# Kernel tuning notes

Measured on AMD Instinct MI355X. Metric: run time of the kernel, lower is better.

## Reference

```python
import jax, jax.numpy as jnp
import numpy as np

INPUT_DIM = 1024
OUTPUT_DIM = 512
N_QUBITS = 12
DEPTH = 8
BATCH = 32768
LN_EPS = 1e-5
NOISE = 0.01


def setup_inputs() -> dict:
    key = jax.random.key(0)
    ks = jax.random.split(key, 12)
    inp = {
        "x": jax.random.normal(ks[0], (BATCH, INPUT_DIM), dtype=jnp.float32),
        "w_in": jax.random.normal(ks[1], (N_QUBITS, INPUT_DIM), dtype=jnp.float32) * 0.03,
        "b_in": jnp.zeros((N_QUBITS,), jnp.float32),
        "ln_g": jnp.ones((N_QUBITS,), jnp.float32),
        "ln_b": jnp.zeros((N_QUBITS,), jnp.float32),
        "rot": jax.random.normal(ks[2], (DEPTH, N_QUBITS, 3), dtype=jnp.float32) * 0.1,
        "ent": jax.random.normal(ks[3], (DEPTH, N_QUBITS - 1), dtype=jnp.float32) * 0.1,
        "w1": jax.random.normal(ks[4], (N_QUBITS, N_QUBITS), dtype=jnp.float32) * 0.3,
        "b1": jnp.zeros((N_QUBITS,), jnp.float32),
        "w2": jax.random.normal(ks[5], (OUTPUT_DIM, N_QUBITS), dtype=jnp.float32) * 0.3,
        "b2": jnp.zeros((OUTPUT_DIM,), jnp.float32),
        "meas_basis": jax.random.normal(ks[6], (N_QUBITS,), dtype=jnp.float32) * 0.1,
    }
    return inp


def _entangle(state, c):
    # c: sigmoid(ent[layer]) shape [n-1]. Effective (traced) torch semantics:
    # out[i]   = s[i]*(1-c_i)   + s[i+1]*c_i     for i in 0..n-2
    # out[n-1] = s[n-1]*(1-c_{n-2}) + s[n-2]*c_{n-2}
    left = state[:, :-1] * (1.0 - c) + state[:, 1:] * c          # [B, n-1]
    last = state[:, -1] * (1.0 - c[-1]) + state[:, -2] * c[-1]   # [B]
    return jnp.concatenate([left, last[:, None]], axis=1)


def reference(x, w_in, b_in, ln_g, ln_b, rot, ent, w1, b1, w2, b2, meas_basis):
    # input layer + layernorm + tanh
    h = x @ w_in.T + b_in                                   # [B, n]
    mu = jnp.mean(h, axis=-1, keepdims=True)
    var = jnp.mean((h - mu) ** 2, axis=-1, keepdims=True)
    h = (h - mu) * jax.lax.rsqrt(var + LN_EPS) * ln_g + ln_b
    h = jnp.tanh(h)

    encoded = h * jnp.float32(np.pi)
    state = jnp.zeros_like(encoded)
    for layer in range(DEPTH):
        rx = encoded + rot[layer, :, 0]
        state = state * jnp.cos(rx * 0.5) + jnp.sin(rot[layer, :, 1] * 0.5)
        state = state * jnp.cos(rot[layer, :, 2] * 0.5)     # Re(exp(i*rz/2))
        if layer < DEPTH - 1:
            state = _entangle(state, jax.nn.sigmoid(ent[layer]))

    # measurement: basis rotation + gaussian noise + tanh
    measured = state * jnp.tanh(meas_basis)
    noise = jax.random.normal(jax.random.key(1234), measured.shape, dtype=measured.dtype) * NOISE
    measured = jnp.tanh(measured + noise)

    # output MLP
    out = jax.nn.relu(measured @ w1.T + b1) @ w2.T + b2     # [B, OUTPUT_DIM]
    return out
```

## Files before the change

kernel.cpp:

```cpp
#include <hip/hip_runtime.h>
#include <cstdint>
#include <cstddef>


__device__ __forceinline__ uint32_t rotl32(uint32_t x, int r) {
  return (x << r) | (x >> (32 - r));
}

__device__ __forceinline__ void threefry2x32(uint32_t k0, uint32_t k1,
                                             uint32_t& x0, uint32_t& x1) {
  const uint32_t k2 = k0 ^ k1 ^ 0x1BD11BDAu;
  x0 += k0; x1 += k1;
#define TF_R(r) { x0 += x1; x1 = rotl32(x1, (r)); x1 ^= x0; }
  TF_R(13) TF_R(15) TF_R(26) TF_R(6)
  x0 += k1; x1 += k2 + 1u;
  TF_R(17) TF_R(29) TF_R(16) TF_R(24)
  x0 += k2; x1 += k0 + 2u;
  TF_R(13) TF_R(15) TF_R(26) TF_R(6)
  x0 += k0; x1 += k1 + 3u;
  TF_R(17) TF_R(29) TF_R(16) TF_R(24)
  x0 += k1; x1 += k2 + 4u;
  TF_R(13) TF_R(15) TF_R(26) TF_R(6)
  x0 += k2; x1 += k0 + 5u;
#undef TF_R
}

__device__ __forceinline__ float erfinv_xla(float x) {
  float w = -log1pf(-x * x);
  float p;
  if (w < 5.0f) {
    w -= 2.5f;
    p = 2.81022636e-08f;
    p = fmaf(p, w, 3.43273939e-07f);
    p = fmaf(p, w, -3.5233877e-06f);
    p = fmaf(p, w, -4.39150654e-06f);
    p = fmaf(p, w, 0.00021858087f);
    p = fmaf(p, w, -0.00125372503f);
    p = fmaf(p, w, -0.00417768164f);
    p = fmaf(p, w, 0.246640727f);
    p = fmaf(p, w, 1.50140941f);
  } else {
    w = sqrtf(w) - 3.0f;
    p = -0.000200214257f;
    p = fmaf(p, w, 0.000100950558f);
    p = fmaf(p, w, 0.00134934322f);
    p = fmaf(p, w, -0.00367342844f);
    p = fmaf(p, w, 0.00573950773f);
    p = fmaf(p, w, -0.0076224613f);
    p = fmaf(p, w, 0.00943887047f);
    p = fmaf(p, w, 1.00167406f);
    p = fmaf(p, w, 2.83297682f);
  }
  return p * x;
}

__global__ __launch_bounds__(256, 3)
void qnn_gemm_in(const float* __restrict__ x, const float* __restrict__ w_in,
                 const float* __restrict__ b_in, float* __restrict__ h) {
  __shared__ float wl[12 * 1024];
  {
    const float4* ws = (const float4*)w_in;
    float4* wd = (float4*)wl;
#pragma unroll
    for (int j = 0; j < 12; ++j) wd[threadIdx.x + 256 * j] = ws[threadIdx.x + 256 * j];
  }
  __syncthreads();

  const int wave = threadIdx.x >> 6;
  const int lane = threadIdx.x & 63;
  const int r    = lane >> 4;
  const int kc   = lane & 15;

  float bq[12];
#pragma unroll
  for (int q = 0; q < 12; ++q) bq[q] = b_in[q];

  for (int it = 0; it < 4; ++it) {
    const int row = (blockIdx.x << 6) + (it << 4) + (wave << 2) + r;
    const float4* xr = (const float4*)(x + (size_t)row * 1024);

    float acc[12];
#pragma unroll
    for (int q = 0; q < 12; ++q) acc[q] = 0.0f;

#pragma unroll 4
    for (int ks = 0; ks < 16; ++ks) {
      const float4 xv = xr[(ks << 4) + kc];
#pragma unroll
      for (int q = 0; q < 12; ++q) {
        const float4 wv = *(const float4*)&wl[q * 1024 + (ks << 6) + (kc << 2)];
        acc[q] += xv.x * wv.x + xv.y * wv.y + xv.z * wv.z + xv.w * wv.w;
      }
    }

#pragma unroll
    for (int q = 0; q < 12; ++q) {
      float v = acc[q];
      v += __shfl_xor(v, 1);
      v += __shfl_xor(v, 2);
      v += __shfl_xor(v, 4);
      v += __shfl_xor(v, 8);
      acc[q] = v + bq[q];
    }
    if (kc == 0) {
      float* hp = h + (size_t)row * 12;
      *(float4*)(hp + 0) = make_float4(acc[0], acc[1], acc[2], acc[3]);
      *(float4*)(hp + 4) = make_float4(acc[4], acc[5], acc[6], acc[7]);
      *(float4*)(hp + 8) = make_float4(acc[8], acc[9], acc[10], acc[11]);
    }
  }
}

__global__ __launch_bounds__(256, 2)
void qnn_tail(const float* __restrict__ h_in,
              const float* __restrict__ ln_g, const float* __restrict__ ln_b,
              const float* __restrict__ rot,  const float* __restrict__ ent,
              const float* __restrict__ w1,   const float* __restrict__ b1,
              const float* __restrict__ w2,   const float* __restrict__ b2,
              const float* __restrict__ meas, float* __restrict__ out) {
  __shared__ float w2s[512 * 12];
  __shared__ float b2s[512];
  __shared__ float hid[64 * 12];
  __shared__ float rot0[8][12], sr1[8][12], cr2[8][12], cen[8][12];
  __shared__ float tmb[12], w1s[144], b1s[12];

  const int t = threadIdx.x;

  {
    const float4* s = (const float4*)w2;
    float4* d = (float4*)w2s;
#pragma unroll
    for (int j = 0; j < 6; ++j) d[t + 256 * j] = s[t + 256 * j];
    if (t < 128) ((float4*)b2s)[t] = ((const float4*)b2)[t];
    if (t < 96) {
      const int l = t / 12, q = t % 12, base = (l * 12 + q) * 3;
      rot0[l][q] = rot[base + 0];
      sr1[l][q]  = sinf(rot[base + 1] * 0.5f);
      cr2[l][q]  = cosf(rot[base + 2] * 0.5f);
    }
    if (t >= 128 && t < 216) {
      const int i = t - 128, l = i / 11, q = i % 11;
      cen[l][q] = 1.0f / (1.0f + expf(-ent[l * 11 + q]));
    }
    if (t >= 216 && t < 228) tmb[t - 216] = tanhf(meas[t - 216]);
    if (t >= 228 && t < 240) b1s[t - 228] = b1[t - 228];
    if (t < 144) w1s[t] = w1[t];
  }
  __syncthreads();

  const int wave = t >> 6, lane = t & 63;
  if (lane < 16) {
    const int rl  = (wave << 4) + lane;
    const int row = (blockIdx.x << 6) + rl;

    const float* hp = h_in + (size_t)row * 12;
    const float4 a0 = *(const float4*)(hp + 0);
    const float4 a1 = *(const float4*)(hp + 4);
    const float4 a2 = *(const float4*)(hp + 8);
    float hv[12] = {a0.x, a0.y, a0.z, a0.w, a1.x, a1.y, a1.z, a1.w,
                    a2.x, a2.y, a2.z, a2.w};

    float s = 0.0f;
#pragma unroll
    for (int q = 0; q < 12; ++q) s += hv[q];
    const float mu = s / 12.0f;
    float var = 0.0f;
#pragma unroll
    for (int q = 0; q < 12; ++q) { const float d = hv[q] - mu; var += d * d; }
    var /= 12.0f;
    const float inv = 1.0f / sqrtf(var + 1e-5f);

    float enc[12];
#pragma unroll
    for (int q = 0; q < 12; ++q) {
      const float n = (hv[q] - mu) * inv * ln_g[q] + ln_b[q];
      enc[q] = tanhf(n) * 3.14159265358979f;
    }

    float st[12];
#pragma unroll
    for (int q = 0; q < 12; ++q) st[q] = 0.0f;
#pragma unroll
    for (int l = 0; l < 8; ++l) {
#pragma unroll
      for (int q = 0; q < 12; ++q) {
        const float rx = enc[q] + rot0[l][q];
        st[q] = st[q] * cosf(rx * 0.5f) + sr1[l][q];
        st[q] *= cr2[l][q];
      }
      if (l < 7) {
        float ns[12];
#pragma unroll
        for (int i = 0; i < 11; ++i) {
          const float c = cen[l][i];
          ns[i] = st[i] * (1.0f - c) + st[i + 1] * c;
        }
        { const float c = cen[l][10]; ns[11] = st[11] * (1.0f - c) + st[10] * c; }
#pragma unroll
        for (int q = 0; q < 12; ++q) st[q] = ns[q];
      }
    }

    const uint32_t base = (uint32_t)row * 12u;
    float m[12];
#pragma unroll
    for (int q = 0; q < 12; ++q) {
      uint32_t x0 = 0u;
      uint32_t x1 = base + (uint32_t)q;
      threefry2x32(0u, 1234u, x0, x1);
      const uint32_t bits = x0 ^ x1;
      const float u01 = __uint_as_float((bits >> 9) | 0x3F800000u) - 1.0f;
      float u = u01 * 2.0f + (-0.99999994f);
      u = fmaxf(-0.99999994f, u);
      const float nrm = 1.41421356237f * erfinv_xla(u);
      m[q] = tanhf(st[q] * tmb[q] + nrm * 0.01f);
    }

    float* hd = &hid[rl * 12];
#pragma unroll
    for (int j = 0; j < 12; ++j) {
      float a = b1s[j];
#pragma unroll
      for (int q = 0; q < 12; ++q) a = fmaf(m[q], w1s[j * 12 + q], a);
      hd[j] = fmaxf(a, 0.0f);
    }
  }
  __syncthreads();

  float wa[12], wb[12];
#pragma unroll
  for (int q = 0; q < 12; ++q) {
    wa[q] = w2s[t * 12 + q];
    wb[q] = w2s[(t + 256) * 12 + q];
  }
  const float ba = b2s[t], bb = b2s[t + 256];
  float* ob = out + (size_t)blockIdx.x * 64 * 512;
  for (int rr = 0; rr < 64; ++rr) {
    const float4 h0 = *(const float4*)&hid[rr * 12 + 0];
    const float4 h1 = *(const float4*)&hid[rr * 12 + 4];
    const float4 h2 = *(const float4*)&hid[rr * 12 + 8];
    const float hvv[12] = {h0.x, h0.y, h0.z, h0.w, h1.x, h1.y, h1.z, h1.w,
                           h2.x, h2.y, h2.z, h2.w};
    float a = ba, b = bb;
#pragma unroll
    for (int q = 0; q < 12; ++q) {
      a = fmaf(hvv[q], wa[q], a);
      b = fmaf(hvv[q], wb[q], b);
    }
    ob[rr * 512 + t] = a;
    ob[rr * 512 + 256 + t] = b;
  }
}

extern "C" void kernel_launch(void* const* d_in, const int* in_sizes, int n_in,
                              void* d_out, int out_size, void* d_ws, size_t ws_size,
                              hipStream_t stream) {
  const float* x    = (const float*)d_in[0];
  const float* w_in = (const float*)d_in[1];
  const float* b_in = (const float*)d_in[2];
  const float* ln_g = (const float*)d_in[3];
  const float* ln_b = (const float*)d_in[4];
  const float* rot  = (const float*)d_in[5];
  const float* ent  = (const float*)d_in[6];
  const float* w1   = (const float*)d_in[7];
  const float* b1   = (const float*)d_in[8];
  const float* w2   = (const float*)d_in[9];
  const float* b2   = (const float*)d_in[10];
  const float* mb   = (const float*)d_in[11];
  float* outp = (float*)d_out;
  float* h    = (float*)d_ws;

  qnn_gemm_in<<<512, 256, 0, stream>>>(x, w_in, b_in, h);
  qnn_tail<<<512, 256, 0, stream>>>(h, ln_g, ln_b, rot, ent, w1, b1, w2, b2, mb, outp);
}
```

Baseline: 292.4 us.

## Parallelize tail per-qubit across lanes and software-pipeline input GEMM loads

The input GEMM now uses 512-thread blocks and issues its x loads early into two alternating register buffers, so global loads overlap the FMA work. The tail kernel switches from one thread per row, with only 16 of 64 lanes active, to 16 lanes per row with one qubit per lane. LayerNorm sums and the entanglement neighbour exchange use wavefront shuffles, and the blocks are halved to 32 rows with twice as many blocks. This targets idle lanes and serial per-row work in the tail, at the cost of extra shuffles, four padded idle lanes per group, and higher register pressure from the prefetch buffers.

```diff
diff --git a/kernel.cpp b/kernel.cpp
--- a/kernel.cpp
+++ b/kernel.cpp
@@ -54,7 +54,7 @@
   return p * x;
 }
 
-__global__ __launch_bounds__(256, 3)
+__global__ __launch_bounds__(512, 4)
 void qnn_gemm_in(const float* __restrict__ x, const float* __restrict__ w_in,
                  const float* __restrict__ b_in, float* __restrict__ h) {
   __shared__ float wl[12 * 1024];
@@ -62,7 +62,7 @@
     const float4* ws = (const float4*)w_in;
     float4* wd = (float4*)wl;
 #pragma unroll
-    for (int j = 0; j < 12; ++j) wd[threadIdx.x + 256 * j] = ws[threadIdx.x + 256 * j];
+    for (int j = 0; j < 6; ++j) wd[threadIdx.x + 512 * j] = ws[threadIdx.x + 512 * j];
   }
   __syncthreads();
 
@@ -75,21 +75,61 @@
 #pragma unroll
   for (int q = 0; q < 12; ++q) bq[q] = b_in[q];
 
-  for (int it = 0; it < 4; ++it) {
-    const int row = (blockIdx.x << 6) + (it << 4) + (wave << 2) + r;
+#pragma unroll
+  for (int it = 0; it < 2; ++it) {
+    const int row = (blockIdx.x << 6) + (wave << 3) + (it << 2) + r;
     const float4* xr = (const float4*)(x + (size_t)row * 1024);
 
+    float4 A[4], B[4];
+#pragma unroll
+    for (int i = 0; i < 4; ++i) A[i] = xr[((0 + i) << 4) + kc];
+#pragma unroll
+    for (int i = 0; i < 4; ++i) B[i] = xr[((4 + i) << 4) + kc];
+
     float acc[12];
 #pragma unroll
     for (int q = 0; q < 12; ++q) acc[q] = 0.0f;
 
-#pragma unroll 4
-    for (int ks = 0; ks < 16; ++ks) {
-      const float4 xv = xr[(ks << 4) + kc];
+#pragma unroll
+    for (int i = 0; i < 4; ++i) {
+      const int ks = i;
 #pragma unroll
       for (int q = 0; q < 12; ++q) {
         const float4 wv = *(const float4*)&wl[q * 1024 + (ks << 6) + (kc << 2)];
-        acc[q] += xv.x * wv.x + xv.y * wv.y + xv.z * wv.z + xv.w * wv.w;
+        acc[q] += A[i].x * wv.x + A[i].y * wv.y + A[i].z * wv.z + A[i].w * wv.w;
+      }
+    }
+#pragma unroll
+    for (int i = 0; i < 4; ++i) A[i] = xr[((8 + i) << 4) + kc];
+
+#pragma unroll
+    for (int i = 0; i < 4; ++i) {
+      const int ks = 4 + i;
+#pragma unroll
+      for (int q = 0; q < 12; ++q) {
+        const float4 wv = *(const float4*)&wl[q * 1024 + (ks << 6) + (kc << 2)];
+        acc[q] += B[i].x * wv.x + B[i].y * wv.y + B[i].z * wv.z + B[i].w * wv.w;
+      }
+    }
+#pragma unroll
+    for (int i = 0; i < 4; ++i) B[i] = xr[((12 + i) << 4) + kc];
+
+#pragma unroll
+    for (int i = 0; i < 4; ++i) {
+      const int ks = 8 + i;
+#pragma unroll
+      for (int q = 0; q < 12; ++q) {
+        const float4 wv = *(const float4*)&wl[q * 1024 + (ks << 6) + (kc << 2)];
+        acc[q] += A[i].x * wv.x + A[i].y * wv.y + A[i].z * wv.z + A[i].w * wv.w;
+      }
+    }
+#pragma unroll
+    for (int i = 0; i < 4; ++i) {
+      const int ks = 12 + i;
+#pragma unroll
+      for (int q = 0; q < 12; ++q) {
+        const float4 wv = *(const float4*)&wl[q * 1024 + (ks << 6) + (kc << 2)];
+        acc[q] += B[i].x * wv.x + B[i].y * wv.y + B[i].z * wv.z + B[i].w * wv.w;
       }
     }
 
@@ -111,7 +151,7 @@
   }
 }
 
-__global__ __launch_bounds__(256, 2)
+__global__ __launch_bounds__(256, 4)
 void qnn_tail(const float* __restrict__ h_in,
               const float* __restrict__ ln_g, const float* __restrict__ ln_b,
               const float* __restrict__ rot,  const float* __restrict__ ent,
@@ -120,9 +160,9 @@
               const float* __restrict__ meas, float* __restrict__ out) {
   __shared__ float w2s[512 * 12];
   __shared__ float b2s[512];
-  __shared__ float hid[64 * 12];
-  __shared__ float rot0[8][12], sr1[8][12], cr2[8][12], cen[8][12];
-  __shared__ float tmb[12], w1s[144], b1s[12];
+  __shared__ float hid[32 * 12];
+  __shared__ float rot0s[8 * 16], sr1s[8 * 16], cr2s[8 * 16], cens[8 * 16];
+  __shared__ float tmbs[16], w1T[12 * 16], b1s[16], lgs[16], lbs[16];
 
   const int t = threadIdx.x;
 
@@ -134,96 +174,19 @@
     if (t < 128) ((float4*)b2s)[t] = ((const float4*)b2)[t];
     if (t < 96) {
       const int l = t / 12, q = t % 12, base = (l * 12 + q) * 3;
-      rot0[l][q] = rot[base + 0];
-      sr1[l][q]  = sinf(rot[base + 1] * 0.5f);
-      cr2[l][q]  = cosf(rot[base + 2] * 0.5f);
-    }
-    if (t >= 128 && t < 216) {
-      const int i = t - 128, l = i / 11, q = i % 11;
-      cen[l][q] = 1.0f / (1.0f + expf(-ent[l * 11 + q]));
-    }
-    if (t >= 216 && t < 228) tmb[t - 216] = tanhf(meas[t - 216]);
-    if (t >= 228 && t < 240) b1s[t - 228] = b1[t - 228];
-    if (t < 144) w1s[t] = w1[t];
-  }
-  __syncthreads();
-
-  const int wave = t >> 6, lane = t & 63;
-  if (lane < 16) {
-    const int rl  = (wave << 4) + lane;
-    const int row = (blockIdx.x << 6) + rl;
-
-    const float* hp = h_in + (size_t)row * 12;
-    const float4 a0 = *(const float4*)(hp + 0);
-    const float4 a1 = *(const float4*)(hp + 4);
-    const float4 a2 = *(const float4*)(hp + 8);
-    float hv[12] = {a0.x, a0.y, a0.z, a0.w, a1.x, a1.y, a1.z, a1.w,
-                    a2.x, a2.y, a2.z, a2.w};
-
-    float s = 0.0f;
-#pragma unroll
-    for (int q = 0; q < 12; ++q) s += hv[q];
-    const float mu = s / 12.0f;
-    float var = 0.0f;
-#pragma unroll
-    for (int q = 0; q < 12; ++q) { const float d = hv[q] - mu; var += d * d; }
-    var /= 12.0f;
-    const float inv = 1.0f / sqrtf(var + 1e-5f);
-
-    float enc[12];
-#pragma unroll
-    for (int q = 0; q < 12; ++q) {
-      const float n = (hv[q] - mu) * inv * ln_g[q] + ln_b[q];
-      enc[q] = tanhf(n) * 3.14159265358979f;
-    }
-
-    float st[12];
-#pragma unroll
-    for (int q = 0; q < 12; ++q) st[q] = 0.0f;
-#pragma unroll
-    for (int l = 0; l < 8; ++l) {
-#pragma unroll
-      for (int q = 0; q < 12; ++q) {
-        const float rx = enc[q] + rot0[l][q];
-        st[q] = st[q] * cosf(rx * 0.5f) + sr1[l][q];
-        st[q] *= cr2[l][q];
-      }
-      if (l < 7) {
-        float ns[12];
-#pragma unroll
-        for (int i = 0; i < 11; ++i) {
-          const float c = cen[l][i];
-          ns[i] = st[i] * (1.0f - c) + st[i + 1] * c;
-        }
-        { const float c = cen[l][10]; ns[11] = st[11] * (1.0f - c) + st[10] * c; }
-#pragma unroll
-        for (int q = 0; q < 12; ++q) st[q] = ns[q];
-      }
-    }
-
-    const uint32_t base = (uint32_t)row * 12u;
-    float m[12];
-#pragma unroll
-    for (int q = 0; q < 12; ++q) {
-      uint32_t x0 = 0u;
-      uint32_t x1 = base + (uint32_t)q;
-      threefry2x32(0u, 1234u, x0, x1);
-      const uint32_t bits = x0 ^ x1;
-      const float u01 = __uint_as_float((bits >> 9) | 0x3F800000u) - 1.0f;
-      float u = u01 * 2.0f + (-0.99999994f);
-      u = fmaxf(-0.99999994f, u);
-      const float nrm = 1.41421356237f * erfinv_xla(u);
-      m[q] = tanhf(st[q] * tmb[q] + nrm * 0.01f);
-    }
-
-    float* hd = &hid[rl * 12];
-#pragma unroll
-    for (int j = 0; j < 12; ++j) {
-      float a = b1s[j];
-#pragma unroll
-      for (int q = 0; q < 12; ++q) a = fmaf(m[q], w1s[j * 12 + q], a);
-      hd[j] = fmaxf(a, 0.0f);
-    }
+      rot0s[l * 16 + q] = rot[base + 0];
+      sr1s[l * 16 + q]  = sinf(rot[base + 1] * 0.5f);
+      cr2s[l * 16 + q]  = cosf(rot[base + 2] * 0.5f);
+    }
+    if (t >= 96 && t < 184) {
+      const int i = t - 96, l = i / 11, q = i % 11;
+      cens[l * 16 + q] = 1.0f / (1.0f + expf(-ent[l * 11 + q]));
+    }
+    if (t >= 184 && t < 196) tmbs[t - 184] = tanhf(meas[t - 184]);
+    if (t >= 196 && t < 208) b1s[t - 196] = b1[t - 196];
+    if (t >= 208 && t < 220) lgs[t - 208] = ln_g[t - 208];
+    if (t >= 220 && t < 232) lbs[t - 220] = ln_b[t - 220];
+    if (t < 144) { const int j = t / 12, q = t % 12; w1T[q * 16 + j] = w1[t]; }
   }
   __syncthreads();
 
@@ -234,8 +197,71 @@
     wb[q] = w2s[(t + 256) * 12 + q];
   }
   const float ba = b2s[t], bb = b2s[t + 256];
-  float* ob = out + (size_t)blockIdx.x * 64 * 512;
-  for (int rr = 0; rr < 64; ++rr) {
+
+  const int lane = t & 63;
+  const int wv   = t >> 6;
+  const int grp  = lane >> 4;
+  const int q    = lane & 15;
+  const int gb   = lane & 48;
+  const bool act = (q < 12);
+  const int cidx = (q == 11) ? 10 : q;
+
+#pragma unroll
+  for (int pass = 0; pass < 2; ++pass) {
+    const int rl  = (pass << 4) + (wv << 2) + grp;
+    const int row = (blockIdx.x << 5) + rl;
+
+    float hq = act ? h_in[(size_t)row * 12 + q] : 0.0f;
+
+    float s = hq;
+    s += __shfl_xor(s, 1); s += __shfl_xor(s, 2);
+    s += __shfl_xor(s, 4); s += __shfl_xor(s, 8);
+    const float mu = s * (1.0f / 12.0f);
+    float d = act ? (hq - mu) : 0.0f;
+    float v2 = d * d;
+    v2 += __shfl_xor(v2, 1); v2 += __shfl_xor(v2, 2);
+    v2 += __shfl_xor(v2, 4); v2 += __shfl_xor(v2, 8);
+    const float inv = 1.0f / sqrtf(v2 * (1.0f / 12.0f) + 1e-5f);
+
+    const float n   = d * inv * lgs[q] + lbs[q];
+    const float enc = tanhf(n) * 3.14159265358979f;
+
+    float st = 0.0f;
+#pragma unroll
+    for (int l = 0; l < 8; ++l) {
+      const float rx = enc + rot0s[l * 16 + q];
+      st = st * cosf(rx * 0.5f) + sr1s[l * 16 + q];
+      st *= cr2s[l * 16 + q];
+      if (l < 7) {
+        const float stn = __shfl(st, lane + 1);
+        const float stp = __shfl(st, lane - 1);
+        const float c   = cens[l * 16 + cidx];
+        const float other = (q == 11) ? stp : stn;
+        st = st * (1.0f - c) + other * c;
+      }
+    }
+
+    uint32_t x0 = 0u, x1 = (uint32_t)row * 12u + (uint32_t)q;
+    threefry2x32(0u, 1234u, x0, x1);
+    const uint32_t bits = x0 ^ x1;
+    const float u01 = __uint_as_float((bits >> 9) | 0x3F800000u) - 1.0f;
+    float u = u01 * 2.0f + (-0.99999994f);
+    u = fmaxf(-0.99999994f, u);
+    const float nrm = 1.41421356237f * erfinv_xla(u);
+    const float m = tanhf(st * tmbs[q] + nrm * 0.01f);
+
+    float acc1 = b1s[q];
+#pragma unroll
+    for (int qq = 0; qq < 12; ++qq) {
+      const float mq = __shfl(m, gb + qq);
+      acc1 = fmaf(mq, w1T[qq * 16 + q], acc1);
+    }
+    if (act) hid[rl * 12 + q] = fmaxf(acc1, 0.0f);
+  }
+  __syncthreads();
+
+  float* ob = out + (size_t)blockIdx.x * 32 * 512;
+  for (int rr = 0; rr < 32; ++rr) {
     const float4 h0 = *(const float4*)&hid[rr * 12 + 0];
     const float4 h1 = *(const float4*)&hid[rr * 12 + 4];
     const float4 h2 = *(const float4*)&hid[rr * 12 + 8];
@@ -243,9 +269,9 @@
                            h2.x, h2.y, h2.z, h2.w};
     float a = ba, b = bb;
 #pragma unroll
-    for (int q = 0; q < 12; ++q) {
-      a = fmaf(hvv[q], wa[q], a);
-      b = fmaf(hvv[q], wb[q], b);
+    for (int qq = 0; qq < 12; ++qq) {
+      a = fmaf(hvv[qq], wa[qq], a);
+      b = fmaf(hvv[qq], wb[qq], b);
     }
     ob[rr * 512 + t] = a;
     ob[rr * 512 + 256 + t] = b;
@@ -270,6 +296,6 @@
   float* outp = (float*)d_out;
   float* h    = (float*)d_ws;
 
-  qnn_gemm_in<<<512, 256, 0, stream>>>(x, w_in, b_in, h);
-  qnn_tail<<<512, 256, 0, stream>>>(h, ln_g, ln_b, rot, ent, w1, b1, w2, b2, mb, outp);
-}
+  qnn_gemm_in<<<512, 512, 0, stream>>>(x, w_in, b_in, h);
+  qnn_tail<<<1024, 256, 0, stream>>>(h, ln_g, ln_b, rot, ent, w1, b1, w2, b2, mb, outp);
+}
```

New measurement: 250.0 us. 1.17x faster.
